# Kernel tuning notes

Measured on AMD Instinct MI355X. Metric: run time of the kernel, lower is better.

Reference implementation:

```python
import jax, jax.numpy as jnp
import numpy as np

N, L, D, H, R = 16384, 8, 256, 256, 64  # nodes, chain len, input dim, hidden dim, rel dim


def setup_inputs() -> dict:
    key = jax.random.key(0)
    ks = jax.random.split(key, 10)
    s = 1.0 / np.sqrt(H)
    f32 = jnp.float32
    return {
        "left_chain": jax.random.normal(ks[0], (N, L, D), f32),
        "right_chain": jax.random.normal(ks[1], (N, L, D), f32),
        "rel": jax.random.normal(ks[2], (N, R), f32),
        "Wih_l": jax.random.normal(ks[3], (4 * H, D), f32) * s,
        "Whh_l": jax.random.normal(ks[4], (4 * H, H), f32) * s,
        "bih_l": jnp.zeros((4 * H,), f32),
        "bhh_l": jnp.zeros((4 * H,), f32),
        "Wih_r": jax.random.normal(ks[5], (4 * H, D), f32) * s,
        "Whh_r": jax.random.normal(ks[6], (4 * H, H), f32) * s,
        "bih_r": jnp.zeros((4 * H,), f32),
        "bhh_r": jnp.zeros((4 * H,), f32),
        "Wenc": jax.random.normal(ks[7], (H, 2 * H + R), f32) * s,
        "benc": jnp.zeros((H,), f32),
    }


def _lstm_last(x, Wih, Whh, bih, bhh):
    # x: [N, L, D]; PyTorch LSTM gate order i, f, g, o; zero initial state.
    n = x.shape[0]
    h0 = jnp.zeros((n, Whh.shape[1]), x.dtype)
    b = bih + bhh

    def step(carry, xt):
        h, c = carry
        g = xt @ Wih.T + h @ Whh.T + b  # [N, 4H]
        i, f, gg, o = jnp.split(g, 4, axis=-1)
        c = jax.nn.sigmoid(f) * c + jax.nn.sigmoid(i) * jnp.tanh(gg)
        h = jax.nn.sigmoid(o) * jnp.tanh(c)
        return (h, c), None

    (h, _c), _ = jax.lax.scan(step, (h0, h0), jnp.swapaxes(x, 0, 1))
    return h  # final hidden state [N, H]


def reference(left_chain, right_chain, rel,
              Wih_l, Whh_l, bih_l, bhh_l,
              Wih_r, Whh_r, bih_r, bhh_r,
              Wenc, benc):
    hl = _lstm_last(left_chain, Wih_l, Whh_l, bih_l, bhh_l)   # el(t)
    hr = _lstm_last(right_chain, Wih_r, Whh_r, bih_r, bhh_r)  # er(t)
    con = jnp.concatenate([hl, hr, rel], axis=-1)             # [N, 2H+R]
    return jnp.tanh(con @ Wenc.T + benc)                      # enc(t): [N, H]
```

## Files before the change

kernel.cpp:

```cpp
#include <hip/hip_runtime.h>
#include <hip/hip_fp16.h>

#define N_NODES 16384
#define SEQ_L   8
#define DIM_D   256
#define DIM_H   256
#define DIM_R   64

typedef float    f32x4 __attribute__((ext_vector_type(4)));
typedef _Float16 f16x8 __attribute__((ext_vector_type(8)));
typedef _Float16 f16x4 __attribute__((ext_vector_type(4)));

__device__ __forceinline__ float fsig(float x) {
    return __builtin_amdgcn_rcpf(1.f + __expf(-x));
}
__device__ __forceinline__ float ftanh(float x) {
    return 1.f - 2.f * __builtin_amdgcn_rcpf(1.f + __expf(2.f * x));
}

__device__ __forceinline__ void pack_w(const float* __restrict__ W, _Float16* __restrict__ P,
                                       int n_colgrp, int n_ks, int Kdim,
                                       int t0, int stride) {
    const int total = n_colgrp * n_ks * 64;
    for (int i = t0; i < total; i += stride) {
        int colgrp = i / (n_ks * 64);
        int rem    = i - colgrp * (n_ks * 64);
        int ks     = rem >> 6;
        int lane   = rem & 63;
        int srow   = colgrp * 16 + (lane & 15);
        int sk     = ks * 32 + (lane >> 4) * 8;
        const float* s = W + (size_t)srow * Kdim + sk;
        f32x4 v0 = *(const f32x4*)s;
        f32x4 v1 = *(const f32x4*)(s + 4);
        f16x8 h;
        h[0] = (_Float16)v0[0]; h[1] = (_Float16)v0[1];
        h[2] = (_Float16)v0[2]; h[3] = (_Float16)v0[3];
        h[4] = (_Float16)v1[0]; h[5] = (_Float16)v1[1];
        h[6] = (_Float16)v1[2]; h[7] = (_Float16)v1[3];
        *(f16x8*)&P[(size_t)i * 8] = h;
    }
}

__global__ void prep_kernel(const float* __restrict__ Wih_l, const float* __restrict__ Whh_l,
                            const float* __restrict__ Wih_r, const float* __restrict__ Whh_r,
                            const float* __restrict__ Wenc,  const float* __restrict__ rel,
                            _Float16* __restrict__ pih_l, _Float16* __restrict__ phh_l,
                            _Float16* __restrict__ pih_r, _Float16* __restrict__ phh_r,
                            _Float16* __restrict__ penc,  _Float16* __restrict__ rel16) {
    const int stride = gridDim.x * blockDim.x;
    const int t0 = blockIdx.x * blockDim.x + threadIdx.x;
    pack_w(Wih_l, pih_l, 64, 8, 256, t0, stride);
    pack_w(Whh_l, phh_l, 64, 8, 256, t0, stride);
    pack_w(Wih_r, pih_r, 64, 8, 256, t0, stride);
    pack_w(Whh_r, phh_r, 64, 8, 256, t0, stride);
    pack_w(Wenc,  penc,  16, 18, 576, t0, stride);
    const int nq = (N_NODES * DIM_R) / 8;
    for (int i = t0; i < nq; i += stride) {
        f32x4 v0 = *(const f32x4*)(rel + (size_t)i * 8);
        f32x4 v1 = *(const f32x4*)(rel + (size_t)i * 8 + 4);
        f16x8 h;
        h[0] = (_Float16)v0[0]; h[1] = (_Float16)v0[1];
        h[2] = (_Float16)v0[2]; h[3] = (_Float16)v0[3];
        h[4] = (_Float16)v1[0]; h[5] = (_Float16)v1[1];
        h[6] = (_Float16)v1[2]; h[7] = (_Float16)v1[3];
        *(f16x8*)&rel16[(size_t)i * 8] = h;
    }
}

__global__ __launch_bounds__(512, 2) void lstm_kernel(
    const float* __restrict__ left, const float* __restrict__ right,
    const _Float16* __restrict__ pih_l, const _Float16* __restrict__ phh_l,
    const _Float16* __restrict__ pih_r, const _Float16* __restrict__ phh_r,
    const float* __restrict__ bih_l, const float* __restrict__ bhh_l,
    const float* __restrict__ bih_r, const float* __restrict__ bhh_r,
    _Float16* __restrict__ hl_out, _Float16* __restrict__ hr_out) {

    const int side = blockIdx.y;
    const float*    chain = side ? right : left;
    const _Float16* Pih   = side ? pih_r : pih_l;
    const _Float16* Phh   = side ? phh_r : phh_l;
    const float*    bih   = side ? bih_r : bih_l;
    const float*    bhh   = side ? bhh_r : bhh_l;
    _Float16*       hout  = side ? hr_out : hl_out;

    __shared__ _Float16 lds_x[64 * 256] __attribute__((aligned(16)));
    __shared__ _Float16 lds_h[64 * 256] __attribute__((aligned(16)));

    const int tid  = threadIdx.x;
    const int lane = tid & 63;
    const int wave = tid >> 6;
    const int l15  = lane & 15;
    const int l4   = lane >> 4;
    const int klb  = l4 * 8;
    const int node0 = blockIdx.x * 64;
    const int hid0  = wave * 32;

    const f32x4 FZ = {0.f, 0.f, 0.f, 0.f};

    float bias[4][2];
#pragma unroll
    for (int g = 0; g < 4; ++g)
#pragma unroll
        for (int ht = 0; ht < 2; ++ht) {
            int col = g * 256 + hid0 + ht * 16 + l15;
            bias[g][ht] = bih[col] + bhh[col];
        }

    const int cg0 = wave * 2;

    f32x4 acc[4][4][2];
    f32x4 cst[4][2];
#pragma unroll
    for (int rt = 0; rt < 4; ++rt)
#pragma unroll
        for (int ht = 0; ht < 2; ++ht) cst[rt][ht] = FZ;

    auto do_gemm = [&](const _Float16* lds, const _Float16* P) {
#pragma unroll
        for (int ks = 0; ks < 8; ++ks) {
            const int kk = ks * 32 + klb;
            f16x8 a[4];
#pragma unroll
            for (int rt = 0; rt < 4; ++rt) {
                int row = rt * 16 + l15;
                int off = row * 256 + (kk ^ ((row & 7) << 3));
                a[rt] = *(const f16x8*)&lds[off];
            }
#pragma unroll
            for (int g = 0; g < 4; ++g)
#pragma unroll
                for (int ht = 0; ht < 2; ++ht) {
                    f16x8 b = *(const f16x8*)&P[(((g * 16 + cg0 + ht) * 8 + ks) << 9) + (lane << 3)];
#pragma unroll
                    for (int rt = 0; rt < 4; ++rt)
                        acc[rt][g][ht] = __builtin_amdgcn_mfma_f32_16x16x32_f16(
                            a[rt], b, acc[rt][g][ht], 0, 0, 0);
                }
        }
    };

#pragma unroll 1
    for (int t = 0; t < SEQ_L; ++t) {
#pragma unroll
        for (int it = 0; it < 8; ++it) {
            int e4  = it * 512 + tid;
            int row = e4 >> 6;
            int kq  = (e4 & 63) << 2;
            f32x4 v = __builtin_nontemporal_load((const f32x4*)(chain +
                      (size_t)(node0 + row) * (SEQ_L * DIM_D) + t * DIM_D + kq));
            f16x4 h4;
            h4[0] = (_Float16)v[0]; h4[1] = (_Float16)v[1];
            h4[2] = (_Float16)v[2]; h4[3] = (_Float16)v[3];
            int idx = row * 256 + (kq ^ ((row & 7) << 3));
            *(f16x4*)&lds_x[idx] = h4;
        }
        __syncthreads();

#pragma unroll
        for (int rt = 0; rt < 4; ++rt)
#pragma unroll
            for (int g = 0; g < 4; ++g)
#pragma unroll
                for (int ht = 0; ht < 2; ++ht) acc[rt][g][ht] = FZ;

        do_gemm(lds_x, Pih);
        if (t > 0) do_gemm(lds_h, Phh);
        __syncthreads();

#pragma unroll
        for (int rt = 0; rt < 4; ++rt)
#pragma unroll
            for (int ht = 0; ht < 2; ++ht)
#pragma unroll
                for (int r = 0; r < 4; ++r) {
                    float gi = acc[rt][0][ht][r] + bias[0][ht];
                    float gf = acc[rt][1][ht][r] + bias[1][ht];
                    float gg = acc[rt][2][ht][r] + bias[2][ht];
                    float go = acc[rt][3][ht][r] + bias[3][ht];
                    float ii = fsig(gi), ff = fsig(gf);
                    float gt = ftanh(gg), oo = fsig(go);
                    float c = ff * cst[rt][ht][r] + ii * gt;
                    cst[rt][ht][r] = c;
                    float h = oo * ftanh(c);
                    int rowl = rt * 16 + l4 * 4 + r;
                    int hid  = hid0 + ht * 16 + l15;
                    lds_h[rowl * 256 + (hid ^ ((rowl & 7) << 3))] = (_Float16)h;
                }
    }

    __syncthreads();
    {
        int row = tid >> 3;
        int seg = (tid & 7) * 32;
        _Float16* dst = hout + (size_t)(node0 + row) * 256 + seg;
        int sw = (row & 7) << 3;
#pragma unroll
        for (int j = 0; j < 4; ++j) {
            f16x8 v = *(const f16x8*)&lds_h[row * 256 + ((seg + j * 8) ^ sw)];
            __builtin_nontemporal_store(v, (f16x8*)(dst + j * 8));
        }
    }
}

__global__ __launch_bounds__(256, 2) void enc_kernel(
    const _Float16* __restrict__ hl, const _Float16* __restrict__ hr,
    const _Float16* __restrict__ rel16, const _Float16* __restrict__ penc,
    const float* __restrict__ benc, float* __restrict__ out) {

    const int tid  = threadIdx.x;
    const int lane = tid & 63;
    const int wave = tid >> 6;
    const int l15  = lane & 15;
    const int l4   = lane >> 4;
    const int klb  = l4 * 8;
    const int row0 = blockIdx.x * 64;
    const int colw = wave * 64;

    const f32x4 FZ = {0.f, 0.f, 0.f, 0.f};
    f32x4 acc[4][4];
#pragma unroll
    for (int rt = 0; rt < 4; ++rt)
#pragma unroll
        for (int ct = 0; ct < 4; ++ct) acc[rt][ct] = FZ;

    float bce[4];
#pragma unroll
    for (int ct = 0; ct < 4; ++ct) bce[ct] = benc[colw + ct * 16 + l15];

    for (int ks = 0; ks < 18; ++ks) {
        const int kk = ks * 32 + klb;
        f16x8 a[4];
#pragma unroll
        for (int rt = 0; rt < 4; ++rt) {
            int row = row0 + rt * 16 + l15;
            const _Float16* p;
            if (ks < 8)       p = hl    + (size_t)row * 256 + kk;
            else if (ks < 16) p = hr    + (size_t)row * 256 + (kk - 256);
            else              p = rel16 + (size_t)row * 64  + (kk - 512);
            a[rt] = *(const f16x8*)p;
        }
#pragma unroll
        for (int ct = 0; ct < 4; ++ct) {
            f16x8 b = *(const f16x8*)&penc[((((wave * 4 + ct) * 18 + ks)) << 9) + (lane << 3)];
#pragma unroll
            for (int rt = 0; rt < 4; ++rt)
                acc[rt][ct] = __builtin_amdgcn_mfma_f32_16x16x32_f16(
                    a[rt], b, acc[rt][ct], 0, 0, 0);
        }
    }

#pragma unroll
    for (int rt = 0; rt < 4; ++rt)
#pragma unroll
        for (int ct = 0; ct < 4; ++ct)
#pragma unroll
            for (int r = 0; r < 4; ++r) {
                int row = row0 + rt * 16 + l4 * 4 + r;
                int col = colw + ct * 16 + l15;
                out[(size_t)row * 256 + col] = ftanh(acc[rt][ct][r] + bce[ct]);
            }
}

extern "C" void kernel_launch(void* const* d_in, const int* in_sizes, int n_in,
                              void* d_out, int out_size, void* d_ws, size_t ws_size,
                              hipStream_t stream) {
    const float* left  = (const float*)d_in[0];
    const float* right = (const float*)d_in[1];
    const float* rel   = (const float*)d_in[2];
    const float* Wih_l = (const float*)d_in[3];
    const float* Whh_l = (const float*)d_in[4];
    const float* bih_l = (const float*)d_in[5];
    const float* bhh_l = (const float*)d_in[6];
    const float* Wih_r = (const float*)d_in[7];
    const float* Whh_r = (const float*)d_in[8];
    const float* bih_r = (const float*)d_in[9];
    const float* bhh_r = (const float*)d_in[10];
    const float* Wenc  = (const float*)d_in[11];
    const float* benc  = (const float*)d_in[12];
    float* out = (float*)d_out;

    char* ws = (char*)d_ws;
    _Float16* pih_l = (_Float16*)(ws);
    _Float16* phh_l = (_Float16*)(ws + 512 * 1024);
    _Float16* pih_r = (_Float16*)(ws + 1024 * 1024);
    _Float16* phh_r = (_Float16*)(ws + 1536 * 1024);
    _Float16* penc  = (_Float16*)(ws + 2048 * 1024);
    _Float16* rel16 = (_Float16*)(ws + 2560 * 1024);
    _Float16* hl16  = (_Float16*)(ws + 4608 * 1024);
    _Float16* hr16  = (_Float16*)(ws + 4608 * 1024 + 8192 * 1024);
    (void)in_sizes; (void)n_in; (void)out_size; (void)ws_size;

    hipLaunchKernelGGL(prep_kernel, dim3(512), dim3(256), 0, stream,
                       Wih_l, Whh_l, Wih_r, Whh_r, Wenc, rel,
                       pih_l, phh_l, pih_r, phh_r, penc, rel16);

    hipLaunchKernelGGL(lstm_kernel, dim3(N_NODES / 64, 2), dim3(512), 0, stream,
                       left, right, pih_l, phh_l, pih_r, phh_r,
                       bih_l, bhh_l, bih_r, bhh_r, hl16, hr16);

    hipLaunchKernelGGL(enc_kernel, dim3(N_NODES / 64), dim3(256), 0, stream,
                       hl16, hr16, rel16, penc, benc, out);
}
```

Baseline: 1.534 ms.

## Repack weights per-wave contiguous, merge LDS buffers, precompute swizzled A offsets

Weights are repacked so each wave's LSTM and encoder fragments sit in one contiguous slab, addressed from a wave-uniform base via readfirstlane. That allows scalar base pointers and hoisting all eight B loads per k-step ahead of the MFMAs. The two LDS tiles become one array, the XOR swizzle drops from 8 rows to 4, and per-row A offsets are precomputed once. The narrower swizzle may bring back some LDS bank conflicts, and holding eight B fragments in flight raises register pressure under the 512-thread, 2-block launch bounds.

```diff
diff --git a/kernel.cpp b/kernel.cpp
--- a/kernel.cpp
+++ b/kernel.cpp
@@ -16,29 +16,6 @@
 }
 __device__ __forceinline__ float ftanh(float x) {
     return 1.f - 2.f * __builtin_amdgcn_rcpf(1.f + __expf(2.f * x));
-}
-
-__device__ __forceinline__ void pack_w(const float* __restrict__ W, _Float16* __restrict__ P,
-                                       int n_colgrp, int n_ks, int Kdim,
-                                       int t0, int stride) {
-    const int total = n_colgrp * n_ks * 64;
-    for (int i = t0; i < total; i += stride) {
-        int colgrp = i / (n_ks * 64);
-        int rem    = i - colgrp * (n_ks * 64);
-        int ks     = rem >> 6;
-        int lane   = rem & 63;
-        int srow   = colgrp * 16 + (lane & 15);
-        int sk     = ks * 32 + (lane >> 4) * 8;
-        const float* s = W + (size_t)srow * Kdim + sk;
-        f32x4 v0 = *(const f32x4*)s;
-        f32x4 v1 = *(const f32x4*)(s + 4);
-        f16x8 h;
-        h[0] = (_Float16)v0[0]; h[1] = (_Float16)v0[1];
-        h[2] = (_Float16)v0[2]; h[3] = (_Float16)v0[3];
-        h[4] = (_Float16)v1[0]; h[5] = (_Float16)v1[1];
-        h[6] = (_Float16)v1[2]; h[7] = (_Float16)v1[3];
-        *(f16x8*)&P[(size_t)i * 8] = h;
-    }
 }
 
 __global__ void prep_kernel(const float* __restrict__ Wih_l, const float* __restrict__ Whh_l,
@@ -49,11 +26,54 @@
                             _Float16* __restrict__ penc,  _Float16* __restrict__ rel16) {
     const int stride = gridDim.x * blockDim.x;
     const int t0 = blockIdx.x * blockDim.x + threadIdx.x;
-    pack_w(Wih_l, pih_l, 64, 8, 256, t0, stride);
-    pack_w(Whh_l, phh_l, 64, 8, 256, t0, stride);
-    pack_w(Wih_r, pih_r, 64, 8, 256, t0, stride);
-    pack_w(Whh_r, phh_r, 64, 8, 256, t0, stride);
-    pack_w(Wenc,  penc,  16, 18, 576, t0, stride);
+
+    const float* SW[4] = {Wih_l, Whh_l, Wih_r, Whh_r};
+    _Float16*    DW[4] = {pih_l, phh_l, pih_r, phh_r};
+    for (int m = 0; m < 4; ++m) {
+        const float* W = SW[m];
+        _Float16*    P = DW[m];
+        for (int i8 = t0; i8 < 32768; i8 += stride) {
+            int w    = i8 >> 12;
+            int rem  = i8 & 4095;
+            int f    = rem >> 6;
+            int lane = rem & 63;
+            int g    = f >> 4;
+            int ht   = (f >> 3) & 1;
+            int ks   = f & 7;
+            int col  = g * 256 + w * 32 + ht * 16 + (lane & 15);
+            int k    = ks * 32 + (lane >> 4) * 8;
+            const float* s = W + (size_t)col * 256 + k;
+            f32x4 v0 = *(const f32x4*)s;
+            f32x4 v1 = *(const f32x4*)(s + 4);
+            f16x8 h;
+            h[0] = (_Float16)v0[0]; h[1] = (_Float16)v0[1];
+            h[2] = (_Float16)v0[2]; h[3] = (_Float16)v0[3];
+            h[4] = (_Float16)v1[0]; h[5] = (_Float16)v1[1];
+            h[6] = (_Float16)v1[2]; h[7] = (_Float16)v1[3];
+            *(f16x8*)&P[(size_t)i8 * 8] = h;
+        }
+    }
+
+    for (int i8 = t0; i8 < 18432; i8 += stride) {
+        int w    = i8 / 4608;
+        int rem  = i8 - w * 4608;
+        int f    = rem >> 6;
+        int lane = rem & 63;
+        int ct   = f / 18;
+        int ks   = f - ct * 18;
+        int col  = w * 64 + ct * 16 + (lane & 15);
+        int k    = ks * 32 + (lane >> 4) * 8;
+        const float* s = Wenc + (size_t)col * 576 + k;
+        f32x4 v0 = *(const f32x4*)s;
+        f32x4 v1 = *(const f32x4*)(s + 4);
+        f16x8 h;
+        h[0] = (_Float16)v0[0]; h[1] = (_Float16)v0[1];
+        h[2] = (_Float16)v0[2]; h[3] = (_Float16)v0[3];
+        h[4] = (_Float16)v1[0]; h[5] = (_Float16)v1[1];
+        h[6] = (_Float16)v1[2]; h[7] = (_Float16)v1[3];
+        *(f16x8*)&penc[(size_t)i8 * 8] = h;
+    }
+
     const int nq = (N_NODES * DIM_R) / 8;
     for (int i = t0; i < nq; i += stride) {
         f32x4 v0 = *(const f32x4*)(rel + (size_t)i * 8);
@@ -77,23 +97,24 @@
 
     const int side = blockIdx.y;
     const float*    chain = side ? right : left;
-    const _Float16* Pih   = side ? pih_r : pih_l;
-    const _Float16* Phh   = side ? phh_r : phh_l;
     const float*    bih   = side ? bih_r : bih_l;
     const float*    bhh   = side ? bhh_r : bhh_l;
     _Float16*       hout  = side ? hr_out : hl_out;
 
-    __shared__ _Float16 lds_x[64 * 256] __attribute__((aligned(16)));
-    __shared__ _Float16 lds_h[64 * 256] __attribute__((aligned(16)));
+    __shared__ _Float16 lds[2 * 64 * 256] __attribute__((aligned(16)));
 
     const int tid  = threadIdx.x;
     const int lane = tid & 63;
     const int wave = tid >> 6;
+    const int wu   = __builtin_amdgcn_readfirstlane(wave);
     const int l15  = lane & 15;
     const int l4   = lane >> 4;
     const int klb  = l4 * 8;
     const int node0 = blockIdx.x * 64;
-    const int hid0  = wave * 32;
+    const int hid0  = wu * 32;
+
+    const _Float16* Pih = (side ? pih_r : pih_l) + wu * 32768;
+    const _Float16* Phh = (side ? phh_r : phh_l) + wu * 32768;
 
     const f32x4 FZ = {0.f, 0.f, 0.f, 0.f};
 
@@ -106,8 +127,6 @@
             bias[g][ht] = bih[col] + bhh[col];
         }
 
-    const int cg0 = wave * 2;
-
     f32x4 acc[4][4][2];
     f32x4 cst[4][2];
 #pragma unroll
@@ -115,27 +134,32 @@
 #pragma unroll
         for (int ht = 0; ht < 2; ++ht) cst[rt][ht] = FZ;
 
-    auto do_gemm = [&](const _Float16* lds, const _Float16* P) {
+    int abase[4];
+#pragma unroll
+    for (int rt = 0; rt < 4; ++rt) {
+        int row = rt * 16 + l15;
+        abase[rt] = row * 256 + (klb ^ ((row & 3) << 3));
+    }
+
+    auto do_gemm = [&](const int lds_ofs, const _Float16* Pw) {
 #pragma unroll
         for (int ks = 0; ks < 8; ++ks) {
-            const int kk = ks * 32 + klb;
             f16x8 a[4];
 #pragma unroll
-            for (int rt = 0; rt < 4; ++rt) {
-                int row = rt * 16 + l15;
-                int off = row * 256 + (kk ^ ((row & 7) << 3));
-                a[rt] = *(const f16x8*)&lds[off];
-            }
+            for (int rt = 0; rt < 4; ++rt)
+                a[rt] = *(const f16x8*)&lds[lds_ofs + abase[rt] + ks * 32];
+            f16x8 b[8];
+#pragma unroll
+            for (int f = 0; f < 8; ++f)
+                b[f] = *(const f16x8*)&Pw[(f * 8 + ks) * 512 + (lane << 3)];
 #pragma unroll
             for (int g = 0; g < 4; ++g)
 #pragma unroll
-                for (int ht = 0; ht < 2; ++ht) {
-                    f16x8 b = *(const f16x8*)&P[(((g * 16 + cg0 + ht) * 8 + ks) << 9) + (lane << 3)];
+                for (int ht = 0; ht < 2; ++ht)
 #pragma unroll
                     for (int rt = 0; rt < 4; ++rt)
                         acc[rt][g][ht] = __builtin_amdgcn_mfma_f32_16x16x32_f16(
-                            a[rt], b, acc[rt][g][ht], 0, 0, 0);
-                }
+                            a[rt], b[g * 2 + ht], acc[rt][g][ht], 0, 0, 0);
         }
     };
 
@@ -151,8 +175,7 @@
             f16x4 h4;
             h4[0] = (_Float16)v[0]; h4[1] = (_Float16)v[1];
             h4[2] = (_Float16)v[2]; h4[3] = (_Float16)v[3];
-            int idx = row * 256 + (kq ^ ((row & 7) << 3));
-            *(f16x4*)&lds_x[idx] = h4;
+            *(f16x4*)&lds[row * 256 + (kq ^ ((row & 3) << 3))] = h4;
         }
         __syncthreads();
 
@@ -163,8 +186,8 @@
 #pragma unroll
                 for (int ht = 0; ht < 2; ++ht) acc[rt][g][ht] = FZ;
 
-        do_gemm(lds_x, Pih);
-        if (t > 0) do_gemm(lds_h, Phh);
+        do_gemm(0, Pih);
+        if (t > 0) do_gemm(16384, Phh);
         __syncthreads();
 
 #pragma unroll
@@ -184,7 +207,7 @@
                     float h = oo * ftanh(c);
                     int rowl = rt * 16 + l4 * 4 + r;
                     int hid  = hid0 + ht * 16 + l15;
-                    lds_h[rowl * 256 + (hid ^ ((rowl & 7) << 3))] = (_Float16)h;
+                    lds[16384 + rowl * 256 + (hid ^ ((rowl & 3) << 3))] = (_Float16)h;
                 }
     }
 
@@ -193,10 +216,10 @@
         int row = tid >> 3;
         int seg = (tid & 7) * 32;
         _Float16* dst = hout + (size_t)(node0 + row) * 256 + seg;
-        int sw = (row & 7) << 3;
+        int sw = (row & 3) << 3;
 #pragma unroll
         for (int j = 0; j < 4; ++j) {
-            f16x8 v = *(const f16x8*)&lds_h[row * 256 + ((seg + j * 8) ^ sw)];
+            f16x8 v = *(const f16x8*)&lds[16384 + row * 256 + ((seg + j * 8) ^ sw)];
             __builtin_nontemporal_store(v, (f16x8*)(dst + j * 8));
         }
     }
@@ -210,11 +233,14 @@
     const int tid  = threadIdx.x;
     const int lane = tid & 63;
     const int wave = tid >> 6;
+    const int wu   = __builtin_amdgcn_readfirstlane(wave);
     const int l15  = lane & 15;
     const int l4   = lane >> 4;
     const int klb  = l4 * 8;
     const int row0 = blockIdx.x * 64;
-    const int colw = wave * 64;
+    const int colw = wu * 64;
+
+    const _Float16* Pw = penc + wu * 36864;
 
     const f32x4 FZ = {0.f, 0.f, 0.f, 0.f};
     f32x4 acc[4][4];
@@ -241,7 +267,7 @@
         }
 #pragma unroll
         for (int ct = 0; ct < 4; ++ct) {
-            f16x8 b = *(const f16x8*)&penc[((((wave * 4 + ct) * 18 + ks)) << 9) + (lane << 3)];
+            f16x8 b = *(const f16x8*)&Pw[(ct * 18 + ks) * 512 + (lane << 3)];
 #pragma unroll
             for (int rt = 0; rt < 4; ++rt)
                 acc[rt][ct] = __builtin_amdgcn_mfma_f32_16x16x32_f16(
```

After: 1.401 ms. 1.1x faster.
